# Kernel optimization log

Hardware: AMD Instinct MI355X
Metric: run time of the kernel (lower is better)

## Reference

```python
import jax, jax.numpy as jnp
import numpy as np

N = 50000      # num nodes
E = 800000     # num edges
F_IN = 100     # input features (ogbn-products)
HID = 128      # hidden_dim (per-head out_channels)
H = 2          # heads
OUT = 47       # num classes
NEG_SLOPE = 0.2


def setup_inputs() -> dict:
    key = jax.random.key(0)
    ks = jax.random.split(key, 14)
    def glorot(k, shape, fan):
        return jax.random.normal(k, shape, jnp.float32) * (1.0 / np.sqrt(fan))
    x = jax.random.normal(ks[0], (N, F_IN), jnp.float32)
    edge_index = jax.random.randint(ks[1], (2, E), 0, N)
    # GAT layer 0: lin_l (= lin_r, shared) weight [H*HID, F_IN], attention vecs [H, HID]
    W0 = glorot(ks[2], (H * HID, F_IN), F_IN)
    b0 = jnp.zeros((H * HID,), jnp.float32)
    attl0 = glorot(ks[3], (H, HID), HID)
    attr0 = glorot(ks[4], (H, HID), HID)
    # GAT layer 1: input dim H*HID
    W1 = glorot(ks[5], (H * HID, H * HID), H * HID)
    b1 = jnp.zeros((H * HID,), jnp.float32)
    attl1 = glorot(ks[6], (H, HID), HID)
    attr1 = glorot(ks[7], (H, HID), HID)
    # post_mp: Linear(H*HID -> HID), Linear(HID -> OUT)
    Wp1 = glorot(ks[8], (HID, H * HID), H * HID)
    bp1 = jnp.zeros((HID,), jnp.float32)
    Wp2 = glorot(ks[9], (OUT, HID), HID)
    bp2 = jnp.zeros((OUT,), jnp.float32)
    return dict(x=x, edge_index=edge_index, W0=W0, b0=b0, attl0=attl0, attr0=attr0,
                W1=W1, b1=b1, attl1=attl1, attr1=attr1,
                Wp1=Wp1, bp1=bp1, Wp2=Wp2, bp2=bp2)


def gat_layer(x, W, b, att_l, att_r, src, dst):
    # shared lin_l == lin_r in the source
    h = (x @ W.T + b).reshape(-1, H, HID)          # [N, H, C]
    alpha_l = jnp.einsum('nhc,hc->nh', h, att_l)   # per-node left scores
    alpha_r = jnp.einsum('nhc,hc->nh', h, att_r)   # per-node right scores
    e = jax.nn.leaky_relu(alpha_l[src] + alpha_r[dst], NEG_SLOPE)  # [E, H]
    # segment softmax over edges grouped by destination node
    emax = jax.ops.segment_max(e, dst, num_segments=N)             # [N, H]
    ee = jnp.exp(e - emax[dst])
    denom = jax.ops.segment_sum(ee, dst, num_segments=N)           # [N, H]
    a = ee / denom[dst]                                            # [E, H]
    msg = a[:, :, None] * h[src]                                   # [E, H, C]
    out = jax.ops.segment_sum(msg, dst, num_segments=N)            # [N, H, C]
    return out.reshape(-1, H * HID)


def reference(x, edge_index, W0, b0, attl0, attr0, W1, b1, attl1, attr1, Wp1, bp1, Wp2, bp2):
    src, dst = edge_index[0], edge_index[1]
    x = jax.nn.relu(gat_layer(x, W0, b0, attl0, attr0, src, dst))
    x = jax.nn.relu(gat_layer(x, W1, b1, attl1, attr1, src, dst))
    h = x @ Wp1.T + bp1           # dropout p=0.0 -> identity
    logits = h @ Wp2.T + bp2
    return jax.nn.log_softmax(logits, axis=1)
```

## Files before the change

### kernel.cpp

```cpp
#include <hip/hip_runtime.h>
#include <math.h>

#define N_NODES 50000
#define E_EDGES 800000
#define F_IN 100
#define HID 128
#define HEADS 2
#define OUT_C 47
#define HH (HEADS*HID)
#define MPAD 50176
#define SLOTS 64

typedef float floatx4 __attribute__((ext_vector_type(4)));
typedef float float2v __attribute__((ext_vector_type(2)));
typedef short short8 __attribute__((ext_vector_type(8)));

__device__ inline ushort bf16round(float v) {
    unsigned u = __float_as_uint(v);
    return (ushort)((u + 0x7FFFu + ((u >> 16) & 1u)) >> 16);
}

__device__ __forceinline__ void gl_lds16(const void* g, void* l) {
    __builtin_amdgcn_global_load_lds(
        (const __attribute__((address_space(1))) unsigned int*)g,
        (__attribute__((address_space(3))) unsigned int*)l, 16, 0, 0);
}

__device__ __forceinline__ void gemm_body(
    int bx, int by,
    const ushort* __restrict__ Ab, const ushort* __restrict__ Wb,
    const float* __restrict__ bias,
    ushort* __restrict__ Hb,
    const float* __restrict__ attl, const float* __restrict__ attr,
    float* __restrict__ al, float* __restrict__ ar,
    int M, int Kp, ushort* sA, ushort* sB)
{
    const int t = threadIdx.x;
    const int wave = t >> 6, lane = t & 63;
    const int quad = lane >> 4, l16 = lane & 15;
    const int rl = lane >> 2, seg = lane & 3;
    const int m0 = by * 64, n0 = bx * 128;

    floatx4 acc[8];
#pragma unroll
    for (int j = 0; j < 8; j++) acc[j] = (floatx4)(0.f);

    for (int k0 = 0; k0 < Kp; k0 += 32) {
        {
            size_t gro = (size_t)(m0 + wave * 16 + rl) * Kp + k0 + seg * 8;
            gl_lds16(Ab + gro, sA + (wave * 16) * 32);
        }
#pragma unroll
        for (int j = 0; j < 2; j++) {
            int br = wave * 32 + j * 16;
            size_t gro = (size_t)(n0 + br + rl) * Kp + k0 + seg * 8;
            gl_lds16(Wb + gro, sB + br * 32);
        }
        __syncthreads();

        short8 af = *(const short8*)(sA + (wave * 16 + l16) * 32 + quad * 8);
#pragma unroll
        for (int sn = 0; sn < 8; sn++) {
            int r = sn * 16 + l16;
            short8 b = *(const short8*)(sB + r * 32 + quad * 8);
            acc[sn] = __builtin_amdgcn_mfma_f32_16x16x32_bf16(af, b, acc[sn], 0, 0, 0);
        }
        __syncthreads();
    }

    float bias_r[8], att_l[8], att_r[8];
#pragma unroll
    for (int sn = 0; sn < 8; sn++) {
        int ai = n0 + sn * 16 + l16;
        bias_r[sn] = bias[ai];
        att_l[sn] = attl[ai];
        att_r[sn] = attr[ai];
    }
#pragma unroll
    for (int r = 0; r < 4; r++) {
        int gm = m0 + wave * 16 + quad * 4 + r;
        float suml = 0.f, sumr = 0.f;
#pragma unroll
        for (int sn = 0; sn < 8; sn++) {
            float v = acc[sn][r] + bias_r[sn];
            suml += v * att_l[sn];
            sumr += v * att_r[sn];
            if (gm < M) {
                int gn = n0 + sn * 16 + l16;
                Hb[(size_t)gm * 256 + gn] = bf16round(v);
            }
        }
#pragma unroll
        for (int off = 1; off < 16; off <<= 1) {
            suml += __shfl_xor(suml, off);
            sumr += __shfl_xor(sumr, off);
        }
        if (l16 == 0 && gm < M) {
            al[gm * HEADS + bx] = suml;
            ar[gm * HEADS + bx] = sumr;
        }
    }
}

__global__ void prep(int* __restrict__ deg,
                     const float* __restrict__ x,  const float* __restrict__ W0,
                     const float* __restrict__ W1, const float* __restrict__ Wp1,
                     const float* __restrict__ Wp2,
                     ushort* __restrict__ xb,  ushort* __restrict__ W0b,
                     ushort* __restrict__ W1b, ushort* __restrict__ Wp1b,
                     ushort* __restrict__ Wp2b) {
    const int cx = N_NODES * 32;
    const int c0 = cx + 256 * 32;
    const int c1 = c0 + (HH * HH) / 4;
    const int c2 = c1 + (HID * HH) / 4;
    const int c3 = c2 + (64 * HID) / 4;
    int i = blockIdx.x * 256 + threadIdx.x;
    if (i < N_NODES) deg[i] = 0;
    if (i >= c3) return;
    float4 v = make_float4(0.f, 0.f, 0.f, 0.f);
    ushort* H; size_t o;
    if (i < cx) {
        int row = i >> 5, kc = (i & 31) * 4;
        if (kc < F_IN) v = *(const float4*)(x + (size_t)row * F_IN + kc);
        H = xb; o = (size_t)row * 128 + kc;
    } else if (i < c0) {
        int j = i - cx;
        int row = j >> 5, kc = (j & 31) * 4;
        if (kc < F_IN) v = *(const float4*)(W0 + (size_t)row * F_IN + kc);
        H = W0b; o = (size_t)row * 128 + kc;
    } else if (i < c1) {
        int j = i - c0;
        v = *(const float4*)(W1 + (size_t)j * 4);
        H = W1b; o = (size_t)j * 4;
    } else if (i < c2) {
        int j = i - c1;
        v = *(const float4*)(Wp1 + (size_t)j * 4);
        H = Wp1b; o = (size_t)j * 4;
    } else {
        int j = i - c2;
        int row = j >> 5;
        if (row < OUT_C) v = *(const float4*)(Wp2 + (size_t)j * 4);
        H = Wp2b; o = (size_t)j * 4;
    }
    ushort4 r;
    r.x = bf16round(v.x); r.y = bf16round(v.y);
    r.z = bf16round(v.z); r.w = bf16round(v.w);
    *(ushort4*)(H + o) = r;
}

#define NG 1568
#define NEB 3136
__global__ __launch_bounds__(256) void gemm_l0_edges(
    const ushort* __restrict__ xb, const ushort* __restrict__ W0b,
    const float* __restrict__ b0,
    const float* __restrict__ attl0, const float* __restrict__ attr0,
    ushort* __restrict__ hb, float* __restrict__ al, float* __restrict__ ar,
    const int* __restrict__ srcv, const int* __restrict__ dstv,
    int* __restrict__ deg, ushort* __restrict__ csr16)
{
    __shared__ ushort sA[64 * 32], sB[128 * 32];
    const int g = blockIdx.x;
    if (g % 3 == 0) {
        const int gm = g / 3;
        const int bx = (gm >> 3) & 1;
        const int by = (gm >> 4) * 8 + (gm & 7);
        gemm_body(bx, by, xb, W0b, b0,
                  hb, attl0, attr0, al, ar, N_NODES, 128, sA, sB);
    } else {
        const int eidx = g - (g + 2) / 3;
        int e = eidx * 256 + threadIdx.x;
        if (e < E_EDGES) {
            int d = dstv[e];
            int r = atomicAdd(&deg[d], 1);
            if (r < SLOTS) csr16[(size_t)d * SLOTS + r] = (ushort)srcv[e];
        }
    }
}

__global__ __launch_bounds__(256) void gemm_l1(
    const ushort* __restrict__ Ab, const ushort* __restrict__ Wb,
    const float* __restrict__ bias, ushort* __restrict__ Hb,
    const float* __restrict__ attl, const float* __restrict__ attr,
    float* __restrict__ al, float* __restrict__ ar)
{
    __shared__ ushort sA[64 * 32], sB[128 * 32];
    const int g = blockIdx.x;
    const int bx = (g >> 3) & 1;
    const int by = (g >> 4) * 8 + (g & 7);
    gemm_body(bx, by, Ab, Wb, bias,
              Hb, attl, attr, al, ar, N_NODES, HH, sA, sB);
}

__global__ __launch_bounds__(256) void gat_aggregate(
    const ushort* __restrict__ hb, const float* __restrict__ al, const float* __restrict__ ar,
    const int* __restrict__ deg, const ushort* __restrict__ csr16,
    ushort* __restrict__ outb)
{
    const int g = blockIdx.x;
    const int xcd = g & 7;
    const int head = xcd & 1;
    const int rank = (g >> 3) * 4 + (xcd >> 1);
    const int wave = threadIdx.x >> 6;
    const int node = rank * 4 + wave;
    const int lane = threadIdx.x & 63;
    const int grp = lane >> 4, c = lane & 15;
    const int n = min(deg[node], SLOTS);
    const float ard = ar[node * HEADS + head];
    const ushort* __restrict__ hbh = hb + head * HID + c * 8;

    float dsum = 0.f;
    float2v av[4];
#pragma unroll
    for (int j = 0; j < 4; j++) av[j] = (float2v)(0.f);

    int s = 0; float w = 0.f;
    if (lane < n) {
        s = (int)csr16[(size_t)node * SLOTS + lane];
        float e = al[s * HEADS + head] + ard;
        e = fmaxf(e, 0.f) + 0.2f * fminf(e, 0.f);
        w = __expf(e);
        dsum = w;
    }
    const int nn = (n + 7) & ~7;
    for (int i = 0; i < nn; i += 8) {
        int e0 = i + grp, e1 = i + 4 + grp;
        int   s0 = __shfl(s, e0);
        float w0 = __shfl(w, e0);
        int   s1 = __shfl(s, e1);
        float w1 = __shfl(w, e1);
        uint4 q0 = *(const uint4*)(hbh + (size_t)s0 * 256);
        uint4 q1 = *(const uint4*)(hbh + (size_t)s1 * 256);
        float2v we0 = (float2v)(w0);
        float2v we1 = (float2v)(w1);
        float2v p;
        p.x = __uint_as_float(q0.x << 16); p.y = __uint_as_float(q0.x & 0xFFFF0000u);
        av[0] += we0 * p;
        p.x = __uint_as_float(q0.y << 16); p.y = __uint_as_float(q0.y & 0xFFFF0000u);
        av[1] += we0 * p;
        p.x = __uint_as_float(q0.z << 16); p.y = __uint_as_float(q0.z & 0xFFFF0000u);
        av[2] += we0 * p;
        p.x = __uint_as_float(q0.w << 16); p.y = __uint_as_float(q0.w & 0xFFFF0000u);
        av[3] += we0 * p;
        p.x = __uint_as_float(q1.x << 16); p.y = __uint_as_float(q1.x & 0xFFFF0000u);
        av[0] += we1 * p;
        p.x = __uint_as_float(q1.y << 16); p.y = __uint_as_float(q1.y & 0xFFFF0000u);
        av[1] += we1 * p;
        p.x = __uint_as_float(q1.z << 16); p.y = __uint_as_float(q1.z & 0xFFFF0000u);
        av[2] += we1 * p;
        p.x = __uint_as_float(q1.w << 16); p.y = __uint_as_float(q1.w & 0xFFFF0000u);
        av[3] += we1 * p;
    }
#pragma unroll
    for (int j = 0; j < 4; j++) {
        av[j].x += __shfl_xor(av[j].x, 16);
        av[j].y += __shfl_xor(av[j].y, 16);
        av[j].x += __shfl_xor(av[j].x, 32);
        av[j].y += __shfl_xor(av[j].y, 32);
    }
#pragma unroll
    for (int off = 32; off; off >>= 1) dsum += __shfl_xor(dsum, off);

    if (grp == 0) {
        const float inv = (n > 0) ? 1.f / dsum : 0.f;
        ushort r[8];
#pragma unroll
        for (int j = 0; j < 4; j++) {
            r[2*j]   = bf16round(fmaxf(av[j].x * inv, 0.f));
            r[2*j+1] = bf16round(fmaxf(av[j].y * inv, 0.f));
        }
        *(uint4*)(outb + (size_t)node * 256 + head * HID + c * 8) = *(uint4*)r;
    }
}

__global__ __launch_bounds__(256) void fused_post(
    const ushort* __restrict__ Ab,
    const ushort* __restrict__ Bb,
    const float* __restrict__ bp1,
    const ushort* __restrict__ W2b,
    const float* __restrict__ bp2,
    float* __restrict__ out, int M)
{
    __shared__ ushort sA[64 * 32];
    __shared__ ushort sB[128 * 32];
    __shared__ ushort sP[64 * 136];

    const int t = threadIdx.x;
    const int wave = t >> 6, lane = t & 63;
    const int quad = lane >> 4, l16 = lane & 15;
    const int rl = lane >> 2, seg = lane & 3;
    const int m0 = blockIdx.x * 64;

    floatx4 acc[8];
#pragma unroll
    for (int j = 0; j < 8; j++) acc[j] = (floatx4)(0.f);

    for (int k0 = 0; k0 < HH; k0 += 32) {
        {
            size_t gro = (size_t)(m0 + wave * 16 + rl) * HH + k0 + seg * 8;
            gl_lds16(Ab + gro, sA + (wave * 16) * 32);
        }
#pragma unroll
        for (int j = 0; j < 2; j++) {
            int br = wave * 32 + j * 16;
            size_t gro = (size_t)(br + rl) * HH + k0 + seg * 8;
            gl_lds16(Bb + gro, sB + br * 32);
        }
        __syncthreads();
        short8 af = *(const short8*)(sA + (wave * 16 + l16) * 32 + quad * 8);
#pragma unroll
        for (int sn = 0; sn < 8; sn++) {
            short8 b = *(const short8*)(sB + (sn * 16 + l16) * 32 + quad * 8);
            acc[sn] = __builtin_amdgcn_mfma_f32_16x16x32_bf16(af, b, acc[sn], 0, 0, 0);
        }
        __syncthreads();
    }
#pragma unroll
    for (int sn = 0; sn < 8; sn++)
#pragma unroll
        for (int r = 0; r < 4; r++) {
            int row = wave * 16 + quad * 4 + r;
            int col = sn * 16 + l16;
            sP[row * 136 + col] = bf16round(acc[sn][r] + bp1[col]);
        }
    __syncthreads();

    floatx4 acc2[4];
#pragma unroll
    for (int j = 0; j < 4; j++) acc2[j] = (floatx4)(0.f);

    for (int k0 = 0; k0 < HID; k0 += 32) {
        {
            int br = wave * 16;
            size_t gro = (size_t)(br + rl) * HID + k0 + seg * 8;
            gl_lds16(W2b + gro, sA + br * 32);
        }
        __syncthreads();
        short8 ph = *(const short8*)(sP + (wave * 16 + l16) * 136 + k0 + quad * 8);
#pragma unroll
        for (int sn = 0; sn < 4; sn++) {
            short8 b = *(const short8*)(sA + (sn * 16 + l16) * 32 + quad * 8);
            acc2[sn] = __builtin_amdgcn_mfma_f32_16x16x32_bf16(ph, b, acc2[sn], 0, 0, 0);
        }
        __syncthreads();
    }

    float b2[4];
#pragma unroll
    for (int sn = 0; sn < 4; sn++) {
        int n = sn * 16 + l16;
        b2[sn] = (n < OUT_C) ? bp2[n] : 0.f;
    }
#pragma unroll
    for (int r = 0; r < 4; r++) {
        float v[4];
        float m = -INFINITY;
#pragma unroll
        for (int sn = 0; sn < 4; sn++) {
            int n = sn * 16 + l16;
            float xv = (n < OUT_C) ? acc2[sn][r] + b2[sn] : -INFINITY;
            v[sn] = xv;
            m = fmaxf(m, xv);
        }
#pragma unroll
        for (int off = 1; off < 16; off <<= 1) m = fmaxf(m, __shfl_xor(m, off));
        float ssum = 0.f;
#pragma unroll
        for (int sn = 0; sn < 4; sn++) {
            int n = sn * 16 + l16;
            if (n < OUT_C) ssum += __expf(v[sn] - m);
        }
#pragma unroll
        for (int off = 1; off < 16; off <<= 1) ssum += __shfl_xor(ssum, off);
        float lse = m + logf(ssum);
        int gm = m0 + wave * 16 + quad * 4 + r;
        if (gm < M) {
#pragma unroll
            for (int sn = 0; sn < 4; sn++) {
                int n = sn * 16 + l16;
                if (n < OUT_C) out[(size_t)gm * OUT_C + n] = v[sn] - lse;
            }
        }
    }
}

extern "C" void kernel_launch(void* const* d_in, const int* in_sizes, int n_in,
                              void* d_out, int out_size, void* d_ws, size_t ws_size,
                              hipStream_t stream) {
    const float* x     = (const float*)d_in[0];
    const int*   ei    = (const int*)d_in[1];
    const float* W0    = (const float*)d_in[2];
    const float* b0    = (const float*)d_in[3];
    const float* attl0 = (const float*)d_in[4];
    const float* attr0 = (const float*)d_in[5];
    const float* W1    = (const float*)d_in[6];
    const float* b1    = (const float*)d_in[7];
    const float* attl1 = (const float*)d_in[8];
    const float* attr1 = (const float*)d_in[9];
    const float* Wp1   = (const float*)d_in[10];
    const float* bp1   = (const float*)d_in[11];
    const float* Wp2   = (const float*)d_in[12];
    const float* bp2   = (const float*)d_in[13];
    float* out = (float*)d_out;

    const int Nn = N_NODES, Etot = E_EDGES;
    const int* srcv = ei;
    const int* dstv = ei + Etot;

    char* ws = (char*)d_ws;
    size_t off = 0;
    auto alloc = [&](size_t bytes) -> void* {
        void* p = ws + off;
        off = (off + bytes + 255) & ~(size_t)255;
        return p;
    };
    int*    deg    = (int*)alloc((size_t)Nn * sizeof(int));
    ushort* csr16  = (ushort*)alloc((size_t)Nn * SLOTS * 2);
    float*  al     = (float*)alloc((size_t)Nn * HEADS * sizeof(float));
    float*  ar     = (float*)alloc((size_t)Nn * HEADS * sizeof(float));
    ushort* xb     = (ushort*)alloc((size_t)MPAD * 128 * 2);
    ushort* W0b    = (ushort*)alloc((size_t)HH * 128 * 2);
    ushort* W1b    = (ushort*)alloc((size_t)HH * HH * 2);
    ushort* Wp1b   = (ushort*)alloc((size_t)HID * HH * 2);
    ushort* Wp2b   = (ushort*)alloc((size_t)64 * HID * 2);
    ushort* hb     = (ushort*)alloc((size_t)MPAD * HH * 2);
    ushort* xbb    = (ushort*)alloc((size_t)MPAD * HH * 2);

    {
        const int tot = N_NODES * 32 + 256 * 32 + (HH * HH) / 4 + (HID * HH) / 4 + (64 * HID) / 4;
        prep<<<(tot + 255) / 256, 256, 0, stream>>>(
            deg, x, W0, W1, Wp1, Wp2, xb, W0b, W1b, Wp1b, Wp2b);
    }

    gemm_l0_edges<<<NG + NEB, 256, 0, stream>>>(
        xb, W0b, b0, attl0, attr0, hb, al, ar, srcv, dstv, deg, csr16);

    gat_aggregate<<<25000, 256, 0, stream>>>(hb, al, ar, deg, csr16, xbb);

    gemm_l1<<<2 * (MPAD / 64), 256, 0, stream>>>(xbb, W1b, b1, hb, attl1, attr1, al, ar);

    gat_aggregate<<<25000, 256, 0, stream>>>(hb, al, ar, deg, csr16, xbb);

    fused_post<<<MPAD / 64, 256, 0, stream>>>(xbb, Wp1b, bp1, Wp2b, bp2, out, Nn);
}
```

Before: 287.5 us.

## Fuse x bf16 conversion into layer-0 GEMM and widen GEMM tiles to both heads

The layer-0 GEMM now reads fp32 x directly, rounds it to bf16 and writes it into shared memory, which removes the separate x conversion pass and its intermediate buffer from prep. Both GEMMs now compute all 256 output columns (both heads) per 64-row block, so each A tile is loaded once instead of twice. A shared two-head epilogue writes h and the per-head attention scores. In exchange, accumulators double to 16 per thread, and the synchronous A conversion in layer 0 can no longer use async global-to-LDS loads.

```diff
diff --git a/kernel.cpp b/kernel.cpp
--- a/kernel.cpp
+++ b/kernel.cpp
@@ -10,6 +10,8 @@
 #define HH (HEADS*HID)
 #define MPAD 50176
 #define SLOTS 64
+#define NGEMM0 (MPAD/64)
+#define NEB 3136
 
 typedef float floatx4 __attribute__((ext_vector_type(4)));
 typedef float float2v __attribute__((ext_vector_type(2)));
@@ -26,91 +28,57 @@
         (__attribute__((address_space(3))) unsigned int*)l, 16, 0, 0);
 }
 
-__device__ __forceinline__ void gemm_body(
-    int bx, int by,
-    const ushort* __restrict__ Ab, const ushort* __restrict__ Wb,
+__device__ __forceinline__ void epi2h(
+    const floatx4* acc,
     const float* __restrict__ bias,
-    ushort* __restrict__ Hb,
     const float* __restrict__ attl, const float* __restrict__ attr,
-    float* __restrict__ al, float* __restrict__ ar,
-    int M, int Kp, ushort* sA, ushort* sB)
+    ushort* __restrict__ Hb, float* __restrict__ al, float* __restrict__ ar,
+    int m0, int wave, int lane)
 {
-    const int t = threadIdx.x;
-    const int wave = t >> 6, lane = t & 63;
     const int quad = lane >> 4, l16 = lane & 15;
-    const int rl = lane >> 2, seg = lane & 3;
-    const int m0 = by * 64, n0 = bx * 128;
-
-    floatx4 acc[8];
-#pragma unroll
-    for (int j = 0; j < 8; j++) acc[j] = (floatx4)(0.f);
-
-    for (int k0 = 0; k0 < Kp; k0 += 32) {
-        {
-            size_t gro = (size_t)(m0 + wave * 16 + rl) * Kp + k0 + seg * 8;
-            gl_lds16(Ab + gro, sA + (wave * 16) * 32);
-        }
-#pragma unroll
-        for (int j = 0; j < 2; j++) {
-            int br = wave * 32 + j * 16;
-            size_t gro = (size_t)(n0 + br + rl) * Kp + k0 + seg * 8;
-            gl_lds16(Wb + gro, sB + br * 32);
-        }
-        __syncthreads();
-
-        short8 af = *(const short8*)(sA + (wave * 16 + l16) * 32 + quad * 8);
+#pragma unroll
+    for (int h = 0; h < 2; h++) {
+        float bias_r[8], att_l[8], att_r[8];
 #pragma unroll
         for (int sn = 0; sn < 8; sn++) {
-            int r = sn * 16 + l16;
-            short8 b = *(const short8*)(sB + r * 32 + quad * 8);
-            acc[sn] = __builtin_amdgcn_mfma_f32_16x16x32_bf16(af, b, acc[sn], 0, 0, 0);
-        }
-        __syncthreads();
-    }
-
-    float bias_r[8], att_l[8], att_r[8];
-#pragma unroll
-    for (int sn = 0; sn < 8; sn++) {
-        int ai = n0 + sn * 16 + l16;
-        bias_r[sn] = bias[ai];
-        att_l[sn] = attl[ai];
-        att_r[sn] = attr[ai];
-    }
-#pragma unroll
-    for (int r = 0; r < 4; r++) {
-        int gm = m0 + wave * 16 + quad * 4 + r;
-        float suml = 0.f, sumr = 0.f;
-#pragma unroll
-        for (int sn = 0; sn < 8; sn++) {
-            float v = acc[sn][r] + bias_r[sn];
-            suml += v * att_l[sn];
-            sumr += v * att_r[sn];
-            if (gm < M) {
-                int gn = n0 + sn * 16 + l16;
-                Hb[(size_t)gm * 256 + gn] = bf16round(v);
-            }
-        }
-#pragma unroll
-        for (int off = 1; off < 16; off <<= 1) {
-            suml += __shfl_xor(suml, off);
-            sumr += __shfl_xor(sumr, off);
-        }
-        if (l16 == 0 && gm < M) {
-            al[gm * HEADS + bx] = suml;
-            ar[gm * HEADS + bx] = sumr;
+            int ai = h * 128 + sn * 16 + l16;
+            bias_r[sn] = bias[ai];
+            att_l[sn] = attl[ai];
+            att_r[sn] = attr[ai];
+        }
+#pragma unroll
+        for (int r = 0; r < 4; r++) {
+            int gm = m0 + wave * 16 + quad * 4 + r;
+            float suml = 0.f, sumr = 0.f;
+#pragma unroll
+            for (int sn = 0; sn < 8; sn++) {
+                float v = acc[h * 8 + sn][r] + bias_r[sn];
+                suml += v * att_l[sn];
+                sumr += v * att_r[sn];
+                if (gm < N_NODES) {
+                    int gn = h * 128 + sn * 16 + l16;
+                    Hb[(size_t)gm * 256 + gn] = bf16round(v);
+                }
+            }
+#pragma unroll
+            for (int off = 1; off < 16; off <<= 1) {
+                suml += __shfl_xor(suml, off);
+                sumr += __shfl_xor(sumr, off);
+            }
+            if (l16 == 0 && gm < N_NODES) {
+                al[gm * HEADS + h] = suml;
+                ar[gm * HEADS + h] = sumr;
+            }
         }
     }
 }
 
 __global__ void prep(int* __restrict__ deg,
-                     const float* __restrict__ x,  const float* __restrict__ W0,
-                     const float* __restrict__ W1, const float* __restrict__ Wp1,
-                     const float* __restrict__ Wp2,
-                     ushort* __restrict__ xb,  ushort* __restrict__ W0b,
-                     ushort* __restrict__ W1b, ushort* __restrict__ Wp1b,
-                     ushort* __restrict__ Wp2b) {
-    const int cx = N_NODES * 32;
-    const int c0 = cx + 256 * 32;
+                     const float* __restrict__ W0, const float* __restrict__ W1,
+                     const float* __restrict__ Wp1, const float* __restrict__ Wp2,
+                     ushort* __restrict__ W0b, ushort* __restrict__ W1b,
+                     ushort* __restrict__ Wp1b, ushort* __restrict__ Wp2b) {
+    const int c0 = 256 * 32;
     const int c1 = c0 + (HH * HH) / 4;
     const int c2 = c1 + (HID * HH) / 4;
     const int c3 = c2 + (64 * HID) / 4;
@@ -119,13 +87,8 @@
     if (i >= c3) return;
     float4 v = make_float4(0.f, 0.f, 0.f, 0.f);
     ushort* H; size_t o;
-    if (i < cx) {
+    if (i < c0) {
         int row = i >> 5, kc = (i & 31) * 4;
-        if (kc < F_IN) v = *(const float4*)(x + (size_t)row * F_IN + kc);
-        H = xb; o = (size_t)row * 128 + kc;
-    } else if (i < c0) {
-        int j = i - cx;
-        int row = j >> 5, kc = (j & 31) * 4;
         if (kc < F_IN) v = *(const float4*)(W0 + (size_t)row * F_IN + kc);
         H = W0b; o = (size_t)row * 128 + kc;
     } else if (i < c1) {
@@ -148,26 +111,62 @@
     *(ushort4*)(H + o) = r;
 }
 
-#define NG 1568
-#define NEB 3136
 __global__ __launch_bounds__(256) void gemm_l0_edges(
-    const ushort* __restrict__ xb, const ushort* __restrict__ W0b,
+    const float* __restrict__ x, const ushort* __restrict__ W0b,
     const float* __restrict__ b0,
     const float* __restrict__ attl0, const float* __restrict__ attr0,
     ushort* __restrict__ hb, float* __restrict__ al, float* __restrict__ ar,
     const int* __restrict__ srcv, const int* __restrict__ dstv,
     int* __restrict__ deg, ushort* __restrict__ csr16)
 {
-    __shared__ ushort sA[64 * 32], sB[128 * 32];
+    __shared__ ushort sA[64 * 32];
+    __shared__ ushort sB[256 * 32];
     const int g = blockIdx.x;
-    if (g % 3 == 0) {
-        const int gm = g / 3;
-        const int bx = (gm >> 3) & 1;
-        const int by = (gm >> 4) * 8 + (gm & 7);
-        gemm_body(bx, by, xb, W0b, b0,
-                  hb, attl0, attr0, al, ar, N_NODES, 128, sA, sB);
+    if (g % 5 == 0) {
+        const int by = g / 5;
+        const int t = threadIdx.x;
+        const int wave = t >> 6, lane = t & 63;
+        const int quad = lane >> 4, l16 = lane & 15;
+        const int rl = lane >> 2, seg = lane & 3;
+        const int m0 = by * 64;
+
+        floatx4 acc[16];
+#pragma unroll
+        for (int j = 0; j < 16; j++) acc[j] = (floatx4)(0.f);
+
+        for (int k0 = 0; k0 < 128; k0 += 32) {
+#pragma unroll
+            for (int rnd = 0; rnd < 2; rnd++) {
+                int row = wave * 16 + (lane >> 3) + rnd * 8;
+                int c4 = (lane & 7) * 4;
+                int col = k0 + c4;
+                int gmr = m0 + row;
+                float4 v = make_float4(0.f, 0.f, 0.f, 0.f);
+                if (gmr < N_NODES && col < F_IN)
+                    v = *(const float4*)(x + (size_t)gmr * F_IN + col);
+                ushort4 u;
+                u.x = bf16round(v.x); u.y = bf16round(v.y);
+                u.z = bf16round(v.z); u.w = bf16round(v.w);
+                *(ushort4*)(sA + row * 32 + c4) = u;
+            }
+#pragma unroll
+            for (int j = 0; j < 4; j++) {
+                int br = wave * 64 + j * 16;
+                size_t gro = (size_t)(br + rl) * 128 + k0 + seg * 8;
+                gl_lds16(W0b + gro, sB + br * 32);
+            }
+            __syncthreads();
+            short8 af = *(const short8*)(sA + (wave * 16 + l16) * 32 + quad * 8);
+#pragma unroll
+            for (int sn = 0; sn < 16; sn++) {
+                short8 b = *(const short8*)(sB + (sn * 16 + l16) * 32 + quad * 8);
+                acc[sn] = __builtin_amdgcn_mfma_f32_16x16x32_bf16(af, b, acc[sn], 0, 0, 0);
+            }
+            __syncthreads();
+        }
+        epi2h(acc, b0, attl0, attr0, hb, al, ar, m0, wave, lane);
     } else {
-        const int eidx = g - (g + 2) / 3;
+        const int eidx = g - g / 5 - 1;
         int e = eidx * 256 + threadIdx.x;
         if (e < E_EDGES) {
             int d = dstv[e];
@@ -183,12 +182,39 @@
     const float* __restrict__ attl, const float* __restrict__ attr,
     float* __restrict__ al, float* __restrict__ ar)
 {
-    __shared__ ushort sA[64 * 32], sB[128 * 32];
-    const int g = blockIdx.x;
-    const int bx = (g >> 3) & 1;
-    const int by = (g >> 4) * 8 + (g & 7);
-    gemm_body(bx, by, Ab, Wb, bias,
-              Hb, attl, attr, al, ar, N_NODES, HH, sA, sB);
+    __shared__ ushort sA[64 * 32];
+    __shared__ ushort sB[256 * 32];
+    const int t = threadIdx.x;
+    const int wave = t >> 6, lane = t & 63;
+    const int quad = lane >> 4, l16 = lane & 15;
+    const int rl = lane >> 2, seg = lane & 3;
+    const int m0 = blockIdx.x * 64;
+
+    floatx4 acc[16];
+#pragma unroll
+    for (int j = 0; j < 16; j++) acc[j] = (floatx4)(0.f);
+
+    for (int k0 = 0; k0 < HH; k0 += 32) {
+        {
+            size_t gro = (size_t)(m0 + wave * 16 + rl) * HH + k0 + seg * 8;
+            gl_lds16(Ab + gro, sA + (wave * 16) * 32);
+        }
+#pragma unroll
+        for (int j = 0; j < 4; j++) {
+            int br = wave * 64 + j * 16;
+            size_t gro = (size_t)(br + rl) * HH + k0 + seg * 8;
+            gl_lds16(Wb + gro, sB + br * 32);
+        }
+        __syncthreads();
+        short8 af = *(const short8*)(sA + (wave * 16 + l16) * 32 + quad * 8);
+#pragma unroll
+        for (int sn = 0; sn < 16; sn++) {
+            short8 b = *(const short8*)(sB + (sn * 16 + l16) * 32 + quad * 8);
+            acc[sn] = __builtin_amdgcn_mfma_f32_16x16x32_bf16(af, b, acc[sn], 0, 0, 0);
+        }
+        __syncthreads();
+    }
+    epi2h(acc, bias, attl, attr, Hb, al, ar, m0, wave, lane);
 }
 
 __global__ __launch_bounds__(256) void gat_aggregate(
@@ -417,7 +443,6 @@
     ushort* csr16  = (ushort*)alloc((size_t)Nn * SLOTS * 2);
     float*  al     = (float*)alloc((size_t)Nn * HEADS * sizeof(float));
     float*  ar     = (float*)alloc((size_t)Nn * HEADS * sizeof(float));
-    ushort* xb     = (ushort*)alloc((size_t)MPAD * 128 * 2);
     ushort* W0b    = (ushort*)alloc((size_t)HH * 128 * 2);
     ushort* W1b    = (ushort*)alloc((size_t)HH * HH * 2);
     ushort* Wp1b   = (ushort*)alloc((size_t)HID * HH * 2);
@@ -425,20 +450,16 @@
     ushort* hb     = (ushort*)alloc((size_t)MPAD * HH * 2);
     ushort* xbb    = (ushort*)alloc((size_t)MPAD * HH * 2);
 
-    {
-        const int tot = N_NODES * 32 + 256 * 32 + (HH * HH) / 4 + (HID * HH) / 4 + (64 * HID) / 4;
-        prep<<<(tot + 255) / 256, 256, 0, stream>>>(
-            deg, x, W0, W1, Wp1, Wp2, xb, W0b, W1b, Wp1b, Wp2b);
-    }
-
-    gemm_l0_edges<<<NG + NEB, 256, 0, stream>>>(
-        xb, W0b, b0, attl0, attr0, hb, al, ar, srcv, dstv, deg, csr16);
+    prep<<<196, 256, 0, stream>>>(deg, W0, W1, Wp1, Wp2, W0b, W1b, Wp1b, Wp2b);
+
+    gemm_l0_edges<<<NGEMM0 + NEB, 256, 0, stream>>>(
+        x, W0b, b0, attl0, attr0, hb, al, ar, srcv, dstv, deg, csr16);
 
     gat_aggregate<<<25000, 256, 0, stream>>>(hb, al, ar, deg, csr16, xbb);
 
-    gemm_l1<<<2 * (MPAD / 64), 256, 0, stream>>>(xbb, W1b, b1, hb, attl1, attr1, al, ar);
+    gemm_l1<<<NGEMM0, 256, 0, stream>>>(xbb, W1b, b1, hb, attl1, attr1, al, ar);
 
     gat_aggregate<<<25000, 256, 0, stream>>>(hb, al, ar, deg, csr16, xbb);
 
-    fused_post<<<MPAD / 64, 256, 0, stream>>>(xbb, Wp1b, bp1, Wp2b, bp2, out, Nn);
-}
+    fused_post<<<NGEMM0, 256, 0, stream>>>(xbb, Wp1b, bp1, Wp2b, bp2, out, Nn);
+}
```

New measurement: 284.9 us. No clear change (-0.9%).
